# Performance work log

Hardware: AMD Instinct MI355X
Metric: run time of the kernel (lower is better)

The kernel has to match this reference:

```python
import jax, jax.numpy as jnp
import numpy as np

D_X, D_K, D_V = 1024, 128, 128
B, N = 8, 2048


def setup_inputs() -> dict:
    key = jax.random.key(0)
    ks = jax.random.split(key, 7)
    s = lambda fan_in: 1.0 / np.sqrt(fan_in)
    return {
        "x": jax.random.normal(ks[0], (B, N, D_X), dtype=jnp.float32),
        "w_q": jax.random.uniform(ks[1], (D_K, D_X), jnp.float32, -s(D_X), s(D_X)),
        "b_q": jax.random.uniform(ks[2], (D_K,), jnp.float32, -s(D_X), s(D_X)),
        "w_k": jax.random.uniform(ks[3], (D_K, D_X), jnp.float32, -s(D_X), s(D_X)),
        "b_k": jax.random.uniform(ks[4], (D_K,), jnp.float32, -s(D_X), s(D_X)),
        "w_v": jax.random.uniform(ks[5], (D_V, D_X), jnp.float32, -s(D_X), s(D_X)),
        "b_v": jax.random.uniform(ks[6], (D_V,), jnp.float32, -s(D_X), s(D_X)),
    }


def reference(x, w_q, b_q, w_k, b_k, w_v, b_v):
    # Q is computed in the original module but unused; omit (no effect on output).
    K = jnp.einsum('bnx,kx->bnk', x, w_k) + b_k  # [B,N,d_k]
    V = jnp.einsum('bnx,vx->bnv', x, w_v) + b_v  # [B,N,d_v]
    # logits = K @ V^T / sqrt(d_k)  -> [B,N,N]  (note: K vs V, not Q vs K)
    scale = 1.0 / np.sqrt(D_K).astype(np.float32)
    logits = jnp.einsum('bnk,bmk->bnm', K, V) * scale
    attn = jax.nn.softmax(logits, axis=-1)
    return jnp.einsum('bnm,bmv->bnv', attn, V)
```

## Files before the change

kernel.cpp:

```cpp
#include <hip/hip_runtime.h>
#include <hip/hip_bf16.h>


typedef short s16x8 __attribute__((ext_vector_type(8)));
typedef float f32x4 __attribute__((ext_vector_type(4)));
typedef unsigned short u16;

#define AS1 __attribute__((address_space(1)))
#define AS3 __attribute__((address_space(3)))

__device__ __forceinline__ void gld_lds16(const void* g, void* l) {
  __builtin_amdgcn_global_load_lds((const AS1 unsigned int*)g, (AS3 unsigned int*)l, 16, 0, 0);
}

__device__ __forceinline__ float bf2f(u16 u) {
  unsigned int v = ((unsigned int)u) << 16;
  return __builtin_bit_cast(float, v);
}
__device__ __forceinline__ u16 f2bf(float f) {
  unsigned int u = __builtin_bit_cast(unsigned int, f);
  u += 0x7fffu + ((u >> 16) & 1u);
  return (u16)(u >> 16);
}
__device__ __forceinline__ unsigned pack_bf2(float a, float b) {
  unsigned ua = __builtin_bit_cast(unsigned, a) + 0x8000u;
  unsigned ub = __builtin_bit_cast(unsigned, b) + 0x8000u;
  return __builtin_amdgcn_perm(ub, ua, 0x07060302u);
}

__global__ __launch_bounds__(256, 4) void wconv_kernel(
    const float* __restrict__ wk, const float* __restrict__ wv,
    u16* __restrict__ wbf)
{
  const int e = (blockIdx.x * 256 + threadIdx.x) * 8;
  const float* src = (e < 131072) ? (wk + e) : (wv + (e - 131072));
  float4 a = *(const float4*)src;
  float4 b = *(const float4*)(src + 4);
  union { unsigned u[4]; s16x8 v; } pk;
  pk.u[0] = pack_bf2(a.x, a.y); pk.u[1] = pack_bf2(a.z, a.w);
  pk.u[2] = pack_bf2(b.x, b.y); pk.u[3] = pack_bf2(b.z, b.w);
  *(s16x8*)(wbf + e) = pk.v;
}

__global__ __launch_bounds__(512, 2) void kv_gemm_kernel(
    const float* __restrict__ x, const u16* __restrict__ wbf,
    const float* __restrict__ bk, const float* __restrict__ bv,
    u16* __restrict__ Kout, u16* __restrict__ Vout, u16* __restrict__ VTout)
{
  __shared__ u16 sA[2][8 * 512];
  __shared__ u16 sB[4][32 * 512];

  const int tid  = threadIdx.x;
  const int wave = tid >> 6;
  const int lane = tid & 63;
  const int l16  = lane & 15;
  const int lq   = lane >> 4;
  const int row0 = blockIdx.x * 64;
  const int wr   = wave >> 2;
  const int wc   = wave & 3;

  f32x4 acc[2][4];
  for (int i = 0; i < 2; ++i)
    for (int j = 0; j < 4; ++j) acc[i][j] = (f32x4){0.f, 0.f, 0.f, 0.f};

  const int kc = tid & 7, arow = tid >> 3;
  const float* aSrc = x + (size_t)(row0 + arow) * 1024 + kc * 8;
  const int aSlot = (((arow >> 4) * 2 + (kc >> 2)) * 512) + ((kc & 3) * 16 + (arow & 15)) * 8;

  const u16* bSrc[4];
  for (int i = 0; i < 4; ++i) {
    const int sl = wave + i * 8;
    bSrc[i] = wbf + (size_t)((sl >> 1) * 16 + l16) * 1024 + (sl & 1) * 32 + lq * 8;
  }

  for (int i = 0; i < 4; ++i)
    gld_lds16(bSrc[i], &sB[0][(wave + i * 8) * 512]);
  float4 p0a = *(const float4*)(aSrc);
  float4 p0b = *(const float4*)(aSrc + 4);
  for (int i = 0; i < 4; ++i)
    gld_lds16(bSrc[i] + 64, &sB[1][(wave + i * 8) * 512]);
  float4 p1a = *(const float4*)(aSrc + 64);
  float4 p1b = *(const float4*)(aSrc + 68);

#pragma unroll
  for (int s = 0; s < 16; ++s) {
    const int buf2 = s & 1, buf4 = s & 3;
    {
      union { unsigned u[4]; s16x8 v; } pk;
      pk.u[0] = pack_bf2(p0a.x, p0a.y); pk.u[1] = pack_bf2(p0a.z, p0a.w);
      pk.u[2] = pack_bf2(p0b.x, p0b.y); pk.u[3] = pack_bf2(p0b.z, p0b.w);
      *(s16x8*)(&sA[buf2][aSlot]) = pk.v;
    }
    asm volatile("s_waitcnt lgkmcnt(0)" ::: "memory");
    __builtin_amdgcn_s_barrier();
    if (s == 15) asm volatile("s_waitcnt vmcnt(0)" ::: "memory");
    else         asm volatile("s_waitcnt vmcnt(6)" ::: "memory");
    __builtin_amdgcn_sched_barrier(0);

    if (s + 2 < 16) {
      for (int i = 0; i < 4; ++i)
        gld_lds16(bSrc[i] + (s + 2) * 64, &sB[(s + 2) & 3][(wave + i * 8) * 512]);
    }
    p0a = p1a; p0b = p1b;
    if (s + 2 < 16) {
      p1a = *(const float4*)(aSrc + (s + 2) * 64);
      p1b = *(const float4*)(aSrc + (s + 2) * 64 + 4);
    }

    s16x8 af[2][2], bfr[4][2];
    for (int rb = 0; rb < 2; ++rb)
      for (int ks = 0; ks < 2; ++ks)
        af[rb][ks] = *(const s16x8*)(&sA[buf2][(((wr * 2 + rb) * 2 + ks) * 64 + lane) * 8]);
    for (int cb = 0; cb < 4; ++cb)
      for (int ks = 0; ks < 2; ++ks)
        bfr[cb][ks] = *(const s16x8*)(&sB[buf4][(((wc * 4 + cb) * 2 + ks) * 64 + lane) * 8]);
    for (int rb = 0; rb < 2; ++rb)
      for (int cb = 0; cb < 4; ++cb)
        for (int ks = 0; ks < 2; ++ks)
          acc[rb][cb] = __builtin_amdgcn_mfma_f32_16x16x32_bf16(af[rb][ks], bfr[cb][ks], acc[rb][cb], 0, 0, 0);
  }

  const int  colBase = wc * 64;
  const bool isV = (wc >= 2);
  u16* outN = isV ? Vout : Kout;
  float fbias[4];
  for (int cb = 0; cb < 4; ++cb) {
    const int col = colBase + cb * 16 + l16;
    fbias[cb] = isV ? bv[col - 128] : bk[col];
  }
  for (int rb = 0; rb < 2; ++rb) {
    const int grow0 = row0 + wr * 32 + rb * 16 + lq * 4;
    for (int cb = 0; cb < 4; ++cb) {
      const int gcol = colBase + cb * 16 + l16;
      const int ocol = isV ? (gcol - 128) : gcol;
      union { u16 u[4]; unsigned long long ull; } pk;
      for (int r = 0; r < 4; ++r) {
        u16 h = f2bf(acc[rb][cb][r] + fbias[cb]);
        outN[(size_t)(grow0 + r) * 128 + ocol] = h;
        pk.u[r] = h;
      }
      if (isV) {
        const int bidx = grow0 >> 11;
        const int n    = grow0 & 2047;
        *(unsigned long long*)(VTout + (size_t)bidx * 128 * 2048 + (size_t)ocol * 2048 + n) = pk.ull;
      }
    }
  }
}

__global__ __launch_bounds__(256, 1) void flash_kernel(
    const u16* __restrict__ Kmat, const u16* __restrict__ Vmat,
    const u16* __restrict__ VT, float* __restrict__ out,
    float* __restrict__ Opart, float* __restrict__ lbuf)
{
  __shared__ u16 sV[2][16 * 512];
  __shared__ u16 sVT[2][16 * 512];
  __shared__ u16 sP[128 * 64];

  const int tid  = threadIdx.x;
  const int wave = tid >> 6;
  const int lane = tid & 63;
  const int l16  = lane & 15;
  const int lq   = lane >> 4;
  const int b    = blockIdx.y;
  const int q0   = blockIdx.x * 128;
  const int z    = blockIdx.z;
  const int ntiles = (2048 / gridDim.z) / 64;
  const int mstart = z * (2048 / gridDim.z);
  const float scale = 0.08838834764831845f;

  s16x8 kf[2][4];
  {
    const u16* Kb = Kmat + ((size_t)b * 2048 + q0 + wave * 32 + l16) * 128 + lq * 8;
    for (int rb = 0; rb < 2; ++rb)
      for (int ks = 0; ks < 4; ++ks)
        kf[rb][ks] = *(const s16x8*)(Kb + rb * 2048 + ks * 32);
  }

  const u16* vSrc[4];  const u16* vtSrc[4];
  {
    const u16* Vb  = Vmat + (size_t)b * 2048 * 128;
    const u16* VTb = VT   + (size_t)b * 128 * 2048;
    for (int i = 0; i < 4; ++i) {
      const int sl = wave + i * 4;
      vSrc[i]  = Vb  + (size_t)((sl >> 2) * 16 + l16) * 128 + (sl & 3) * 32 + lq * 8;
      vtSrc[i] = VTb + (size_t)((sl >> 1) * 16 + l16) * 2048 + (sl & 1) * 32 + lq * 8;
    }
  }

  f32x4 oacc[2][8];
  for (int rb = 0; rb < 2; ++rb)
    for (int v = 0; v < 8; ++v) oacc[rb][v] = (f32x4){0.f, 0.f, 0.f, 0.f};
  float lrow[2][4] = {{0.f, 0.f, 0.f, 0.f}, {0.f, 0.f, 0.f, 0.f}};

  for (int i = 0; i < 4; ++i) {
    gld_lds16(vSrc[i] + (size_t)mstart * 128, &sV[0][(wave + i * 4) * 512]);
    gld_lds16(vtSrc[i] + mstart,              &sVT[0][(wave + i * 4) * 512]);
  }

  for (int mt = 0; mt < ntiles; ++mt) {
    const int buf = mt & 1;
    __syncthreads();
    if (mt + 1 < ntiles) {
      const int m1 = mstart + (mt + 1) * 64;
      for (int i = 0; i < 4; ++i) {
        gld_lds16(vSrc[i] + (size_t)m1 * 128, &sV[buf ^ 1][(wave + i * 4) * 512]);
        gld_lds16(vtSrc[i] + m1,              &sVT[buf ^ 1][(wave + i * 4) * 512]);
      }
    }

    f32x4 sacc[2][4];
    for (int rb = 0; rb < 2; ++rb)
      for (int t = 0; t < 4; ++t) sacc[rb][t] = (f32x4){0.f, 0.f, 0.f, 0.f};
    for (int t = 0; t < 4; ++t)
      for (int ks = 0; ks < 4; ++ks) {
        const s16x8 bv = *(const s16x8*)(&sV[buf][(t * 4 + ks) * 512 + lane * 8]);
        sacc[0][t] = __builtin_amdgcn_mfma_f32_16x16x32_bf16(kf[0][ks], bv, sacc[0][t], 0, 0, 0);
        sacc[1][t] = __builtin_amdgcn_mfma_f32_16x16x32_bf16(kf[1][ks], bv, sacc[1][t], 0, 0, 0);
      }

    for (int rb = 0; rb < 2; ++rb)
      for (int r = 0; r < 4; ++r) {
        const int row = wave * 32 + rb * 16 + lq * 4 + r;
        const int xr  = (row & 7) << 3;
        float rs = 0.f;
        for (int t = 0; t < 4; ++t) {
          float p = __expf(sacc[rb][t][r] * scale);
          u16 h = f2bf(p);
          sP[row * 64 + ((t * 16 + l16) ^ xr)] = h;
          rs += bf2f(h);
        }
        lrow[rb][r] += rs;
      }

    for (int ksm = 0; ksm < 2; ++ksm) {
      s16x8 a[2];
      for (int rb = 0; rb < 2; ++rb) {
        const int row = wave * 32 + rb * 16 + l16;
        a[rb] = *(const s16x8*)(&sP[row * 64 + ((ksm * 32 + lq * 8) ^ ((row & 7) << 3))]);
      }
      for (int v = 0; v < 8; ++v) {
        const s16x8 bvt = *(const s16x8*)(&sVT[buf][(v * 2 + ksm) * 512 + lane * 8]);
        oacc[0][v] = __builtin_amdgcn_mfma_f32_16x16x32_bf16(a[0], bvt, oacc[0][v], 0, 0, 0);
        oacc[1][v] = __builtin_amdgcn_mfma_f32_16x16x32_bf16(a[1], bvt, oacc[1][v], 0, 0, 0);
      }
    }
  }

  for (int rb = 0; rb < 2; ++rb)
    for (int r = 0; r < 4; ++r) {
      lrow[rb][r] += __shfl_xor(lrow[rb][r], 1);
      lrow[rb][r] += __shfl_xor(lrow[rb][r], 2);
      lrow[rb][r] += __shfl_xor(lrow[rb][r], 4);
      lrow[rb][r] += __shfl_xor(lrow[rb][r], 8);
    }

  const size_t rowg0 = (size_t)b * 2048 + q0 + wave * 32;
  if (gridDim.z == 1) {
    for (int rb = 0; rb < 2; ++rb)
      for (int r = 0; r < 4; ++r) {
        const float inv = 1.f / lrow[rb][r];
        for (int v = 0; v < 8; ++v)
          out[(rowg0 + rb * 16 + lq * 4 + r) * 128 + v * 16 + l16] = oacc[rb][v][r] * inv;
      }
  } else {
    float* Op = Opart + (size_t)z * 2097152;
    float* lp = lbuf + (size_t)z * 32768;
    for (int rb = 0; rb < 2; ++rb)
      for (int r = 0; r < 4; ++r)
        for (int v = 0; v < 8; ++v)
          Op[(rowg0 + rb * 16 + lq * 4 + r) * 128 + v * 16 + l16] = oacc[rb][v][r];
    if (l16 == 0)
      for (int rb = 0; rb < 2; ++rb)
        for (int r = 0; r < 4; ++r)
          lp[rowg0 + rb * 16 + lq * 4 + r] = lrow[rb][r];
  }
}

__global__ __launch_bounds__(256, 4) void combine_kernel(
    const float* __restrict__ Opart, const float* __restrict__ lbuf,
    float* __restrict__ out)
{
  const int idx = blockIdx.x * 256 + threadIdx.x;
  const int row = idx >> 5;
  const float4 o0 = ((const float4*)Opart)[idx];
  const float4 o1 = ((const float4*)(Opart + 2097152))[idx];
  const float inv = 1.f / (lbuf[row] + lbuf[32768 + row]);
  float4 o;
  o.x = (o0.x + o1.x) * inv;
  o.y = (o0.y + o1.y) * inv;
  o.z = (o0.z + o1.z) * inv;
  o.w = (o0.w + o1.w) * inv;
  ((float4*)out)[idx] = o;
}

extern "C" void kernel_launch(void* const* d_in, const int* in_sizes, int n_in,
                              void* d_out, int out_size, void* d_ws, size_t ws_size,
                              hipStream_t stream) {
  const float* x  = (const float*)d_in[0];
  const float* wk = (const float*)d_in[3];
  const float* bk = (const float*)d_in[4];
  const float* wv = (const float*)d_in[5];
  const float* bv = (const float*)d_in[6];

  u16* ws   = (u16*)d_ws;
  u16* wbf  = ws;
  u16* Kmat = ws + 262144;
  u16* Vmat = Kmat + (size_t)16384 * 128;
  u16* VTm  = Vmat + (size_t)16384 * 128;
  float* Opart = (float*)(VTm + (size_t)16384 * 128);
  float* lbuf  = Opart + 2 * 2097152;
  const bool split = ws_size >= (size_t)30200000;

  wconv_kernel<<<128, 256, 0, stream>>>(wk, wv, wbf);
  kv_gemm_kernel<<<256, 512, 0, stream>>>(x, wbf, bk, bv, Kmat, Vmat, VTm);
  if (split) {
    flash_kernel<<<dim3(16, 8, 2), 256, 0, stream>>>(Kmat, Vmat, VTm,
                                                     (float*)d_out, Opart, lbuf);
    combine_kernel<<<2048, 256, 0, stream>>>(Opart, lbuf, (float*)d_out);
  } else {
    flash_kernel<<<dim3(16, 8, 1), 256, 0, stream>>>(Kmat, Vmat, VTm,
                                                     (float*)d_out, Opart, lbuf);
  }
}
```

Before: 180.7 us.

## Restructure flash kernel into 64-row blocks with split V halves and deeper prefetch

The softmax scale is folded into K when the GEMM epilogue writes it, which removes one multiply per logit. The flash kernel now handles 64 query rows per block, and each pair of waves splits the key/value dimension so that each wave computes half the logits and half the output columns. The key tile drops to 32 and the prefetch ring grows to four buffers with explicit vmcnt waits, setprio around MFMA, and two launches per CU. Per-row sums are merged across the wave pair through LDS, and the grid is doubled. This costs extra barriers per tile and lowers MFMA work per barrier, and rounding K to bf16 after scaling slightly changes numerics.

```diff
diff --git a/kernel.cpp b/kernel.cpp
--- a/kernel.cpp
+++ b/kernel.cpp
@@ -122,6 +122,7 @@
 
   const int  colBase = wc * 64;
   const bool isV = (wc >= 2);
+  const float vscale = isV ? 1.0f : 0.08838834764831845f;
   u16* outN = isV ? Vout : Kout;
   float fbias[4];
   for (int cb = 0; cb < 4; ++cb) {
@@ -135,7 +136,7 @@
       const int ocol = isV ? (gcol - 128) : gcol;
       union { u16 u[4]; unsigned long long ull; } pk;
       for (int r = 0; r < 4; ++r) {
-        u16 h = f2bf(acc[rb][cb][r] + fbias[cb]);
+        u16 h = f2bf((acc[rb][cb][r] + fbias[cb]) * vscale);
         outN[(size_t)(grow0 + r) * 128 + ocol] = h;
         pk.u[r] = h;
       }
@@ -148,103 +149,112 @@
   }
 }
 
-__global__ __launch_bounds__(256, 1) void flash_kernel(
+__global__ __launch_bounds__(256, 2) void flash_kernel(
     const u16* __restrict__ Kmat, const u16* __restrict__ Vmat,
     const u16* __restrict__ VT, float* __restrict__ out,
     float* __restrict__ Opart, float* __restrict__ lbuf)
 {
-  __shared__ u16 sV[2][16 * 512];
-  __shared__ u16 sVT[2][16 * 512];
-  __shared__ u16 sP[128 * 64];
+  __shared__ u16 sV[4][4096];
+  __shared__ u16 sVT[4][4096];
+  __shared__ u16 sP[64 * 40];
+  __shared__ float lred[2][2][32];
 
   const int tid  = threadIdx.x;
   const int wave = tid >> 6;
   const int lane = tid & 63;
   const int l16  = lane & 15;
   const int lq   = lane >> 4;
+  const int qg   = wave >> 1;
+  const int mh   = wave & 1;
   const int b    = blockIdx.y;
-  const int q0   = blockIdx.x * 128;
+  const int q0   = blockIdx.x * 64;
   const int z    = blockIdx.z;
-  const int ntiles = (2048 / gridDim.z) / 64;
-  const int mstart = z * (2048 / gridDim.z);
-  const float scale = 0.08838834764831845f;
+  const int nkv    = 2048 / gridDim.z;
+  const int ntiles = nkv / 32;
+  const int mstart = z * nkv;
 
   s16x8 kf[2][4];
   {
-    const u16* Kb = Kmat + ((size_t)b * 2048 + q0 + wave * 32 + l16) * 128 + lq * 8;
+    const u16* Kb = Kmat + ((size_t)b * 2048 + q0 + qg * 32 + l16) * 128 + lq * 8;
     for (int rb = 0; rb < 2; ++rb)
       for (int ks = 0; ks < 4; ++ks)
         kf[rb][ks] = *(const s16x8*)(Kb + rb * 2048 + ks * 32);
   }
 
-  const u16* vSrc[4];  const u16* vtSrc[4];
+  const u16* Vb  = Vmat + (size_t)b * 2048 * 128;
+  const u16* VTb = VT   + (size_t)b * 128 * 2048;
+  const int sl0 = wave, sl1 = wave + 4;
+  const u16* vS0 = Vb + (size_t)((sl0 >> 2) * 16 + l16) * 128 + (sl0 & 3) * 32 + lq * 8;
+  const u16* vS1 = Vb + (size_t)((sl1 >> 2) * 16 + l16) * 128 + (sl1 & 3) * 32 + lq * 8;
+  const u16* tS0 = VTb + (size_t)(sl0 * 16 + l16) * 2048 + lq * 8;
+  const u16* tS1 = VTb + (size_t)(sl1 * 16 + l16) * 2048 + lq * 8;
+
+  f32x4 oacc[2][4];
+  for (int rb = 0; rb < 2; ++rb)
+    for (int v = 0; v < 4; ++v) oacc[rb][v] = (f32x4){0.f, 0.f, 0.f, 0.f};
+  float lrow[2][4] = {{0.f, 0.f, 0.f, 0.f}, {0.f, 0.f, 0.f, 0.f}};
+
   {
-    const u16* Vb  = Vmat + (size_t)b * 2048 * 128;
-    const u16* VTb = VT   + (size_t)b * 128 * 2048;
-    for (int i = 0; i < 4; ++i) {
-      const int sl = wave + i * 4;
-      vSrc[i]  = Vb  + (size_t)((sl >> 2) * 16 + l16) * 128 + (sl & 3) * 32 + lq * 8;
-      vtSrc[i] = VTb + (size_t)((sl >> 1) * 16 + l16) * 2048 + (sl & 1) * 32 + lq * 8;
-    }
-  }
-
-  f32x4 oacc[2][8];
-  for (int rb = 0; rb < 2; ++rb)
-    for (int v = 0; v < 8; ++v) oacc[rb][v] = (f32x4){0.f, 0.f, 0.f, 0.f};
-  float lrow[2][4] = {{0.f, 0.f, 0.f, 0.f}, {0.f, 0.f, 0.f, 0.f}};
-
-  for (int i = 0; i < 4; ++i) {
-    gld_lds16(vSrc[i] + (size_t)mstart * 128, &sV[0][(wave + i * 4) * 512]);
-    gld_lds16(vtSrc[i] + mstart,              &sVT[0][(wave + i * 4) * 512]);
-  }
-
+    const size_t m0 = (size_t)mstart;
+    gld_lds16(vS0 + m0 * 128, &sV[0][sl0 * 512]);
+    gld_lds16(vS1 + m0 * 128, &sV[0][sl1 * 512]);
+    gld_lds16(tS0 + m0,       &sVT[0][sl0 * 512]);
+    gld_lds16(tS1 + m0,       &sVT[0][sl1 * 512]);
+    const size_t m1 = (size_t)(mstart + 32);
+    gld_lds16(vS0 + m1 * 128, &sV[1][sl0 * 512]);
+    gld_lds16(vS1 + m1 * 128, &sV[1][sl1 * 512]);
+    gld_lds16(tS0 + m1,       &sVT[1][sl0 * 512]);
+    gld_lds16(tS1 + m1,       &sVT[1][sl1 * 512]);
+  }
+
+#pragma unroll 4
   for (int mt = 0; mt < ntiles; ++mt) {
-    const int buf = mt & 1;
-    __syncthreads();
-    if (mt + 1 < ntiles) {
-      const int m1 = mstart + (mt + 1) * 64;
-      for (int i = 0; i < 4; ++i) {
-        gld_lds16(vSrc[i] + (size_t)m1 * 128, &sV[buf ^ 1][(wave + i * 4) * 512]);
-        gld_lds16(vtSrc[i] + m1,              &sVT[buf ^ 1][(wave + i * 4) * 512]);
+    const int buf = mt & 3;
+    asm volatile("s_waitcnt vmcnt(4)" ::: "memory");
+    asm volatile("s_barrier" ::: "memory");
+    __builtin_amdgcn_sched_barrier(0);
+    {
+      int t2 = mt + 2; if (t2 > ntiles - 1) t2 = ntiles - 1;
+      const int bufn = (mt + 2) & 3;
+      const size_t m2 = (size_t)(mstart + t2 * 32);
+      gld_lds16(vS0 + m2 * 128, &sV[bufn][sl0 * 512]);
+      gld_lds16(vS1 + m2 * 128, &sV[bufn][sl1 * 512]);
+      gld_lds16(tS0 + m2,       &sVT[bufn][sl0 * 512]);
+      gld_lds16(tS1 + m2,       &sVT[bufn][sl1 * 512]);
+    }
+    __builtin_amdgcn_sched_barrier(0);
+
+    f32x4 sacc[2];
+    sacc[0] = (f32x4){0.f, 0.f, 0.f, 0.f};
+    sacc[1] = (f32x4){0.f, 0.f, 0.f, 0.f};
+    __builtin_amdgcn_s_setprio(1);
+    for (int ks = 0; ks < 4; ++ks) {
+      const s16x8 bvv = *(const s16x8*)(&sV[buf][(mh * 4 + ks) * 512 + lane * 8]);
+      sacc[0] = __builtin_amdgcn_mfma_f32_16x16x32_bf16(kf[0][ks], bvv, sacc[0], 0, 0, 0);
+      sacc[1] = __builtin_amdgcn_mfma_f32_16x16x32_bf16(kf[1][ks], bvv, sacc[1], 0, 0, 0);
+    }
+    __builtin_amdgcn_s_setprio(0);
+
+    for (int rb = 0; rb < 2; ++rb)
+      for (int r = 0; r < 4; ++r) {
+        float p = __expf(sacc[rb][r]);
+        u16 h = f2bf(p);
+        sP[(qg * 32 + rb * 16 + lq * 4 + r) * 40 + mh * 16 + l16] = h;
+        lrow[rb][r] += bf2f(h);
       }
-    }
-
-    f32x4 sacc[2][4];
-    for (int rb = 0; rb < 2; ++rb)
-      for (int t = 0; t < 4; ++t) sacc[rb][t] = (f32x4){0.f, 0.f, 0.f, 0.f};
-    for (int t = 0; t < 4; ++t)
-      for (int ks = 0; ks < 4; ++ks) {
-        const s16x8 bv = *(const s16x8*)(&sV[buf][(t * 4 + ks) * 512 + lane * 8]);
-        sacc[0][t] = __builtin_amdgcn_mfma_f32_16x16x32_bf16(kf[0][ks], bv, sacc[0][t], 0, 0, 0);
-        sacc[1][t] = __builtin_amdgcn_mfma_f32_16x16x32_bf16(kf[1][ks], bv, sacc[1][t], 0, 0, 0);
-      }
-
-    for (int rb = 0; rb < 2; ++rb)
-      for (int r = 0; r < 4; ++r) {
-        const int row = wave * 32 + rb * 16 + lq * 4 + r;
-        const int xr  = (row & 7) << 3;
-        float rs = 0.f;
-        for (int t = 0; t < 4; ++t) {
-          float p = __expf(sacc[rb][t][r] * scale);
-          u16 h = f2bf(p);
-          sP[row * 64 + ((t * 16 + l16) ^ xr)] = h;
-          rs += bf2f(h);
-        }
-        lrow[rb][r] += rs;
-      }
-
-    for (int ksm = 0; ksm < 2; ++ksm) {
-      s16x8 a[2];
-      for (int rb = 0; rb < 2; ++rb) {
-        const int row = wave * 32 + rb * 16 + l16;
-        a[rb] = *(const s16x8*)(&sP[row * 64 + ((ksm * 32 + lq * 8) ^ ((row & 7) << 3))]);
-      }
-      for (int v = 0; v < 8; ++v) {
-        const s16x8 bvt = *(const s16x8*)(&sVT[buf][(v * 2 + ksm) * 512 + lane * 8]);
-        oacc[0][v] = __builtin_amdgcn_mfma_f32_16x16x32_bf16(a[0], bvt, oacc[0][v], 0, 0, 0);
-        oacc[1][v] = __builtin_amdgcn_mfma_f32_16x16x32_bf16(a[1], bvt, oacc[1][v], 0, 0, 0);
-      }
-    }
+    asm volatile("s_waitcnt lgkmcnt(0)" ::: "memory");
+    asm volatile("s_barrier" ::: "memory");
+
+    s16x8 pa[2];
+    for (int rb = 0; rb < 2; ++rb)
+      pa[rb] = *(const s16x8*)(&sP[(qg * 32 + rb * 16 + l16) * 40 + lq * 8]);
+    __builtin_amdgcn_s_setprio(1);
+    for (int v = 0; v < 4; ++v) {
+      const s16x8 bvt = *(const s16x8*)(&sVT[buf][(mh * 4 + v) * 512 + lane * 8]);
+      oacc[0][v] = __builtin_amdgcn_mfma_f32_16x16x32_bf16(pa[0], bvt, oacc[0][v], 0, 0, 0);
+      oacc[1][v] = __builtin_amdgcn_mfma_f32_16x16x32_bf16(pa[1], bvt, oacc[1][v], 0, 0, 0);
+    }
+    __builtin_amdgcn_s_setprio(0);
   }
 
   for (int rb = 0; rb < 2; ++rb)
@@ -254,26 +264,35 @@
       lrow[rb][r] += __shfl_xor(lrow[rb][r], 4);
       lrow[rb][r] += __shfl_xor(lrow[rb][r], 8);
     }
-
-  const size_t rowg0 = (size_t)b * 2048 + q0 + wave * 32;
+  if (l16 == 0)
+    for (int rb = 0; rb < 2; ++rb)
+      for (int r = 0; r < 4; ++r)
+        lred[qg][mh][rb * 16 + lq * 4 + r] = lrow[rb][r];
+  __syncthreads();
+  float lt[2][4];
+  for (int rb = 0; rb < 2; ++rb)
+    for (int r = 0; r < 4; ++r)
+      lt[rb][r] = lrow[rb][r] + lred[qg][mh ^ 1][rb * 16 + lq * 4 + r];
+
+  const size_t rowg = (size_t)b * 2048 + q0 + qg * 32;
   if (gridDim.z == 1) {
     for (int rb = 0; rb < 2; ++rb)
       for (int r = 0; r < 4; ++r) {
-        const float inv = 1.f / lrow[rb][r];
-        for (int v = 0; v < 8; ++v)
-          out[(rowg0 + rb * 16 + lq * 4 + r) * 128 + v * 16 + l16] = oacc[rb][v][r] * inv;
+        const float inv = 1.f / lt[rb][r];
+        for (int v = 0; v < 4; ++v)
+          out[(rowg + rb * 16 + lq * 4 + r) * 128 + mh * 64 + v * 16 + l16] = oacc[rb][v][r] * inv;
       }
   } else {
     float* Op = Opart + (size_t)z * 2097152;
     float* lp = lbuf + (size_t)z * 32768;
     for (int rb = 0; rb < 2; ++rb)
       for (int r = 0; r < 4; ++r)
-        for (int v = 0; v < 8; ++v)
-          Op[(rowg0 + rb * 16 + lq * 4 + r) * 128 + v * 16 + l16] = oacc[rb][v][r];
-    if (l16 == 0)
+        for (int v = 0; v < 4; ++v)
+          Op[(rowg + rb * 16 + lq * 4 + r) * 128 + mh * 64 + v * 16 + l16] = oacc[rb][v][r];
+    if (mh == 0 && l16 == 0)
       for (int rb = 0; rb < 2; ++rb)
         for (int r = 0; r < 4; ++r)
-          lp[rowg0 + rb * 16 + lq * 4 + r] = lrow[rb][r];
+          lp[rowg + rb * 16 + lq * 4 + r] = lt[rb][r];
   }
 }
 
@@ -315,11 +334,11 @@
   wconv_kernel<<<128, 256, 0, stream>>>(wk, wv, wbf);
   kv_gemm_kernel<<<256, 512, 0, stream>>>(x, wbf, bk, bv, Kmat, Vmat, VTm);
   if (split) {
-    flash_kernel<<<dim3(16, 8, 2), 256, 0, stream>>>(Kmat, Vmat, VTm,
+    flash_kernel<<<dim3(32, 8, 2), 256, 0, stream>>>(Kmat, Vmat, VTm,
                                                      (float*)d_out, Opart, lbuf);
     combine_kernel<<<2048, 256, 0, stream>>>(Opart, lbuf, (float*)d_out);
   } else {
-    flash_kernel<<<dim3(16, 8, 1), 256, 0, stream>>>(Kmat, Vmat, VTm,
+    flash_kernel<<<dim3(32, 8, 1), 256, 0, stream>>>(Kmat, Vmat, VTm,
                                                      (float*)d_out, Opart, lbuf);
   }
 }
```

New measurement: 173.1 us. 4.2% less time.
